# Optimization experiments

Measured on AMD Instinct MI355X. Metric: run time of the kernel, lower is better.

## Reference

```python
import jax, jax.numpy as jnp
import numpy as np

IN_F, OUT_F, RANK, ALPHA, NUM_ADAPTERS = 1024, 1024, 8, 1.0, 8
B, S = 32, 1024
SCALE = ALPHA / RANK


def setup_inputs() -> dict:
    key = jax.random.key(0)
    k1, k2, k3, k4, k5, k6 = jax.random.split(key, 6)
    x = jax.random.normal(k1, (B, S, IN_F), dtype=jnp.float32)
    subject_id = jax.random.randint(k2, (B,), 0, NUM_ADAPTERS)
    # base linear: W [out,in], bias [out] (torch nn.Linear layout)
    W = jax.random.normal(k3, (OUT_F, IN_F), dtype=jnp.float32) * (1.0 / np.sqrt(IN_F))
    b = jax.random.normal(k4, (OUT_F,), dtype=jnp.float32) * 0.01
    # stacked LoRA weights: A [E, rank, in], Bw [E, out, rank]
    # (original inits Bw to zeros; randomized here so the LoRA path is exercised)
    A = jax.random.normal(k5, (NUM_ADAPTERS, RANK, IN_F), dtype=jnp.float32) * 0.02
    Bw = jax.random.normal(k6, (NUM_ADAPTERS, OUT_F, RANK), dtype=jnp.float32) * 0.02
    return {"x": x, "W": W, "b": b, "A": A, "Bw": Bw, "subject_id": subject_id}


def reference(x, W, b, A, Bw, subject_id):
    # base linear: [B,S,O]
    out = jnp.einsum("bsd,od->bso", x, W) + b
    # gather per-batch adapter weights (equivalent to the per-adapter mask loop)
    A_sel = A[subject_id]   # [B, rank, in]
    B_sel = Bw[subject_id]  # [B, out, rank]
    h = jnp.einsum("bsd,brd->bsr", x, A_sel)          # [B,S,rank]
    lora = jnp.einsum("bsr,bor->bso", h, B_sel) * SCALE  # [B,S,out]
    return out + lora
```

## Files before the change

kernel.cpp:

```cpp
#include <hip/hip_runtime.h>
#include <hip/hip_bf16.h>

typedef __bf16 bf16_t;
typedef bf16_t bf16x4 __attribute__((ext_vector_type(4)));
typedef bf16_t bf16x8 __attribute__((ext_vector_type(8)));
typedef float  f32x4  __attribute__((ext_vector_type(4)));

#define IN_F   1024
#define OUT_F  1024
#define RANK   8
#define NE     8
#define BATCH  32
#define SEQ    1024
#define M_TOT  (BATCH * SEQ)
#define SCALE  0.125f
#define NT     16

#define GLOAD_LDS16(g, l)                                                     \
  __builtin_amdgcn_global_load_lds(                                           \
      (const __attribute__((address_space(1))) void*)(g),                     \
      (__attribute__((address_space(3))) void*)(l), 16, 0, 0)

#define CFENCE asm volatile("" ::: "memory")
#define BAR()                                                                 \
  do { CFENCE; __builtin_amdgcn_s_barrier(); CFENCE; } while (0)
#define VMCNT(n) asm volatile("s_waitcnt vmcnt(" #n ")" ::: "memory")

__global__ __launch_bounds__(256) void build_weff(
    const float* __restrict__ W, const float* __restrict__ A,
    const float* __restrict__ Bw, bf16_t* __restrict__ weff) {
  const int e  = blockIdx.x >> 10;
  const int o  = blockIdx.x & 1023;
  const int d0 = threadIdx.x << 2;

  f32x4 acc = *(const f32x4*)(W + ((size_t)o << 10) + d0);
  const float* bwr = Bw + (((size_t)e << 10) + o) * RANK;
  const float* ab  = A + (((size_t)e * RANK) << 10) + d0;
#pragma unroll
  for (int r = 0; r < RANK; ++r) {
    const float s = SCALE * bwr[r];
    const f32x4 a4 = *(const f32x4*)(ab + ((size_t)r << 10));
    acc += s * a4;
  }
  bf16x4 ov;
#pragma unroll
  for (int j = 0; j < 4; ++j) ov[j] = (bf16_t)acc[j];
  *(bf16x4*)(weff + (((size_t)e << 10) + o) * IN_F + d0) = ov;
}

__global__ __launch_bounds__(256) void cvt_x(const float* __restrict__ x,
                                             bf16_t* __restrict__ xb, int n4) {
  int i = blockIdx.x * 256 + threadIdx.x;
  const int stride = gridDim.x * 256;
  for (; i < n4; i += stride) {
    const f32x4 v = *(const f32x4*)(x + ((size_t)i << 2));
    bf16x4 o;
#pragma unroll
    for (int j = 0; j < 4; ++j) o[j] = (bf16_t)v[j];
    *(bf16x4*)(xb + ((size_t)i << 2)) = o;
  }
}

__global__ __launch_bounds__(512, 2) void gemm256(
    const bf16_t* __restrict__ xb, const bf16_t* __restrict__ weff,
    const float* __restrict__ bias, const int* __restrict__ sid,
    float* __restrict__ out) {
  __shared__ bf16_t lds[2][2][2][8192];

  const int bid0 = blockIdx.x;
  const int wgid = ((bid0 & 7) << 6) + (bid0 >> 3);
  const int mb = wgid >> 2, nb = wgid & 3;
  const int m0 = mb << 8, n0 = nb << 8;
  const int e = sid[mb >> 2];

  const int tid = threadIdx.x;
  const int lane = tid & 63, wid = tid >> 6;
  const int wm = wid >> 2, wn = wid & 3;

  const bf16_t* agbase = xb + ((size_t)m0 << 10);
  const bf16_t* bgbase = weff + ((size_t)e << 20) + ((size_t)n0 << 10);

  int soff[2];
#pragma unroll
  for (int i = 0; i < 2; ++i) {
    const int r = (wid << 5) + (i << 4) + (lane >> 2);
    const int sg = (lane & 3) ^ ((r >> 1) & 3);
    soff[i] = (r << 10) + (sg << 3);
  }

  int aoff[8], boff[4];
#pragma unroll
  for (int mi = 0; mi < 8; ++mi) {
    const int r = (wm << 7) + (mi << 4) + (lane & 15);
    const int g = (lane >> 4) ^ ((r >> 1) & 3);
    aoff[mi] = (r << 5) + (g << 3);
  }
#pragma unroll
  for (int ni = 0; ni < 4; ++ni) {
    const int r = (wn << 6) + (ni << 4) + (lane & 15);
    const int g = (lane >> 4) ^ ((r >> 1) & 3);
    boff[ni] = (r << 5) + (g << 3);
  }

  f32x4 acc[8][4] = {};

#define STAGE2(kt, kh)                                                        \
  do {                                                                        \
    bf16_t* _da = &lds[(kt) & 1][0][kh][wid << 10];                           \
    bf16_t* _db = &lds[(kt) & 1][1][kh][wid << 10];                           \
    const int _kc = ((kt) << 6) + ((kh) << 5);                                \
    GLOAD_LDS16(agbase + _kc + soff[0], _da);                                 \
    GLOAD_LDS16(agbase + _kc + soff[1], _da + 512);                           \
    GLOAD_LDS16(bgbase + _kc + soff[0], _db);                                 \
    GLOAD_LDS16(bgbase + _kc + soff[1], _db + 512);                           \
  } while (0)

#define PHASE_READS(kt, kh)                                                   \
  do {                                                                        \
    const bf16_t* _ab = &lds[(kt) & 1][0][kh][0];                             \
    const bf16_t* _bb = &lds[(kt) & 1][1][kh][0];                             \
    _Pragma("unroll") for (int mi = 0; mi < 8; ++mi)                          \
        af[mi] = *(const bf16x8*)(_ab + aoff[mi]);                            \
    _Pragma("unroll") for (int ni = 0; ni < 4; ++ni)                          \
        bfr[ni] = *(const bf16x8*)(_bb + boff[ni]);                           \
  } while (0)

#define MFMAS()                                                               \
  do {                                                                        \
    __builtin_amdgcn_s_setprio(1);                                            \
    _Pragma("unroll") for (int mi = 0; mi < 8; ++mi)                          \
        _Pragma("unroll") for (int ni = 0; ni < 4; ++ni)                      \
            acc[mi][ni] = __builtin_amdgcn_mfma_f32_16x16x32_bf16(            \
                af[mi], bfr[ni], acc[mi][ni], 0, 0, 0);                       \
    __builtin_amdgcn_s_setprio(0);                                            \
  } while (0)

  STAGE2(0, 0);
  STAGE2(0, 1);

  bf16x8 af[8], bfr[4];
  for (int j = 0; j < NT - 1; ++j) {
    VMCNT(4);
    BAR();
    PHASE_READS(j, 0);
    STAGE2(j + 1, 0);
    MFMAS();
    VMCNT(4);
    BAR();
    PHASE_READS(j, 1);
    STAGE2(j + 1, 1);
    MFMAS();
  }
  VMCNT(4);
  BAR();
  PHASE_READS(NT - 1, 0);
  MFMAS();
  VMCNT(0);
  BAR();
  PHASE_READS(NT - 1, 1);
  MFMAS();

  const int R0 = m0 + (wm << 7);
  const int C0 = n0 + (wn << 6);
  const int crow = (lane >> 4) << 2;
  const int ccol = lane & 15;
#pragma unroll
  for (int ni = 0; ni < 4; ++ni) {
    const int col = C0 + (ni << 4) + ccol;
    const float bv = bias[col];
#pragma unroll
    for (int mi = 0; mi < 8; ++mi) {
      const int row = R0 + (mi << 4) + crow;
#pragma unroll
      for (int j2 = 0; j2 < 4; ++j2)
        __builtin_nontemporal_store(acc[mi][ni][j2] + bv,
                                    &out[((size_t)(row + j2) << 10) + col]);
    }
  }
#undef STAGE2
#undef PHASE_READS
#undef MFMAS
}

__global__ __launch_bounds__(256) void lora_naive(
    const float* __restrict__ x, const float* __restrict__ W,
    const float* __restrict__ bias, const float* __restrict__ A,
    const float* __restrict__ Bw, const int* __restrict__ sid,
    float* __restrict__ out) {
  const int m = blockIdx.x;
  const int e = sid[m >> 10];
  __shared__ float xs[IN_F];
  __shared__ float h[RANK];
  const int tid = threadIdx.x;
  for (int i = tid; i < IN_F; i += 256) xs[i] = x[((size_t)m << 10) + i];
  __syncthreads();
  if (tid < RANK) {
    float s = 0.f;
    const float* ar = A + (((size_t)e * RANK + tid) << 10);
    for (int d = 0; d < IN_F; ++d) s += xs[d] * ar[d];
    h[tid] = s * SCALE;
  }
  __syncthreads();
  for (int o = tid; o < OUT_F; o += 256) {
    const float* wr = W + ((size_t)o << 10);
    float s = 0.f;
    for (int d = 0; d < IN_F; ++d) s += xs[d] * wr[d];
    const float* bwr = Bw + (((size_t)e << 10) + o) * RANK;
    float l = 0.f;
#pragma unroll
    for (int r = 0; r < RANK; ++r) l += h[r] * bwr[r];
    out[((size_t)m << 10) + o] = s + bias[o] + l;
  }
}

extern "C" void kernel_launch(void* const* d_in, const int* in_sizes, int n_in,
                              void* d_out, int out_size, void* d_ws,
                              size_t ws_size, hipStream_t stream) {
  const float* x   = (const float*)d_in[0];
  const float* W   = (const float*)d_in[1];
  const float* b   = (const float*)d_in[2];
  const float* A   = (const float*)d_in[3];
  const float* Bw  = (const float*)d_in[4];
  const int*   sid = (const int*)d_in[5];
  float* out = (float*)d_out;

  const size_t weff_bytes = (size_t)NE * OUT_F * IN_F * 2;
  const size_t xb_bytes   = (size_t)M_TOT * IN_F * 2;

  if (ws_size >= weff_bytes + xb_bytes) {
    bf16_t* weff = (bf16_t*)d_ws;
    bf16_t* xb   = (bf16_t*)((char*)d_ws + weff_bytes);
    hipLaunchKernelGGL(build_weff, dim3(NE * OUT_F), dim3(256), 0, stream,
                       W, A, Bw, weff);
    hipLaunchKernelGGL(cvt_x, dim3(4096), dim3(256), 0, stream,
                       x, xb, M_TOT * IN_F / 4);
    hipLaunchKernelGGL(gemm256, dim3((M_TOT / 256) * (OUT_F / 256)),
                       dim3(512), 0, stream, xb, weff, b, sid, out);
  } else {
    hipLaunchKernelGGL(lora_naive, dim3(M_TOT), dim3(256), 0, stream,
                       x, W, b, A, Bw, sid, out);
  }
}
```

Before: 128.3 us.

## Merge prep kernels and restructure GEMM main loop into finer-grained staged pipeline

Fuses the weight-building and x-conversion kernels into one launch, cutting one kernel launch and letting the two prep workloads overlap. The GEMM main loop is rewritten as a deeper pipeline: A and B tiles are staged separately, two tiles ahead for B, and the MFMA work is split into four sub-phases that interleave LDS reads, global-to-LDS loads and barriers. The output store changes from nontemporal to a regular store. The extra barriers and the more complex vmcnt accounting add sync overhead and a risk of mis-scheduled waits.

```diff
diff --git a/kernel.cpp b/kernel.cpp
--- a/kernel.cpp
+++ b/kernel.cpp
@@ -26,38 +26,40 @@
   do { CFENCE; __builtin_amdgcn_s_barrier(); CFENCE; } while (0)
 #define VMCNT(n) asm volatile("s_waitcnt vmcnt(" #n ")" ::: "memory")
 
-__global__ __launch_bounds__(256) void build_weff(
+__global__ __launch_bounds__(256) void prep(
     const float* __restrict__ W, const float* __restrict__ A,
-    const float* __restrict__ Bw, bf16_t* __restrict__ weff) {
-  const int e  = blockIdx.x >> 10;
-  const int o  = blockIdx.x & 1023;
-  const int d0 = threadIdx.x << 2;
-
-  f32x4 acc = *(const f32x4*)(W + ((size_t)o << 10) + d0);
-  const float* bwr = Bw + (((size_t)e << 10) + o) * RANK;
-  const float* ab  = A + (((size_t)e * RANK) << 10) + d0;
-#pragma unroll
-  for (int r = 0; r < RANK; ++r) {
-    const float s = SCALE * bwr[r];
-    const f32x4 a4 = *(const f32x4*)(ab + ((size_t)r << 10));
-    acc += s * a4;
-  }
-  bf16x4 ov;
-#pragma unroll
-  for (int j = 0; j < 4; ++j) ov[j] = (bf16_t)acc[j];
-  *(bf16x4*)(weff + (((size_t)e << 10) + o) * IN_F + d0) = ov;
-}
-
-__global__ __launch_bounds__(256) void cvt_x(const float* __restrict__ x,
-                                             bf16_t* __restrict__ xb, int n4) {
-  int i = blockIdx.x * 256 + threadIdx.x;
-  const int stride = gridDim.x * 256;
-  for (; i < n4; i += stride) {
-    const f32x4 v = *(const f32x4*)(x + ((size_t)i << 2));
-    bf16x4 o;
-#pragma unroll
-    for (int j = 0; j < 4; ++j) o[j] = (bf16_t)v[j];
-    *(bf16x4*)(xb + ((size_t)i << 2)) = o;
+    const float* __restrict__ Bw, const float* __restrict__ x,
+    bf16_t* __restrict__ weff, bf16_t* __restrict__ xb) {
+  const int bid = blockIdx.x;
+  if (bid < NE * OUT_F) {
+    const int e  = bid >> 10;
+    const int o  = bid & 1023;
+    const int d0 = threadIdx.x << 2;
+    f32x4 acc = *(const f32x4*)(W + ((size_t)o << 10) + d0);
+    const float* bwr = Bw + (((size_t)e << 10) + o) * RANK;
+    const float* ab  = A + (((size_t)e * RANK) << 10) + d0;
+#pragma unroll
+    for (int r = 0; r < RANK; ++r) {
+      const float s = SCALE * bwr[r];
+      const f32x4 a4 = *(const f32x4*)(ab + ((size_t)r << 10));
+      acc += s * a4;
+    }
+    bf16x4 ov;
+#pragma unroll
+    for (int j = 0; j < 4; ++j) ov[j] = (bf16_t)acc[j];
+    *(bf16x4*)(weff + (((size_t)e << 10) + o) * IN_F + d0) = ov;
+  } else {
+    const int cb = bid - NE * OUT_F;
+    int i = cb * 256 + threadIdx.x;
+    const int stride = 2048 * 256;
+    const int n4 = M_TOT * IN_F / 4;
+    for (; i < n4; i += stride) {
+      const f32x4 v = *(const f32x4*)(x + ((size_t)i << 2));
+      bf16x4 o;
+#pragma unroll
+      for (int j = 0; j < 4; ++j) o[j] = (bf16_t)v[j];
+      *(bf16x4*)(xb + ((size_t)i << 2)) = o;
+    }
   }
 }
 
@@ -65,7 +67,8 @@
     const bf16_t* __restrict__ xb, const bf16_t* __restrict__ weff,
     const float* __restrict__ bias, const int* __restrict__ sid,
     float* __restrict__ out) {
-  __shared__ bf16_t lds[2][2][2][8192];
+  __shared__ bf16_t lds_a[2][2][8192];
+  __shared__ bf16_t lds_b[2][2][8192];
 
   const int bid0 = blockIdx.x;
   const int wgid = ((bid0 & 7) << 6) + (bid0 >> 3);
@@ -103,62 +106,81 @@
   }
 
   f32x4 acc[8][4] = {};
-
-#define STAGE2(kt, kh)                                                        \
-  do {                                                                        \
-    bf16_t* _da = &lds[(kt) & 1][0][kh][wid << 10];                           \
-    bf16_t* _db = &lds[(kt) & 1][1][kh][wid << 10];                           \
+  bf16x8 afq[4], bf0[4], bf1[4];
+
+#define ASTG(kt, c, kh)                                                       \
+  do {                                                                        \
+    bf16_t* _d = &lds_a[c][kh][wid << 10];                                    \
     const int _kc = ((kt) << 6) + ((kh) << 5);                                \
-    GLOAD_LDS16(agbase + _kc + soff[0], _da);                                 \
-    GLOAD_LDS16(agbase + _kc + soff[1], _da + 512);                           \
-    GLOAD_LDS16(bgbase + _kc + soff[0], _db);                                 \
-    GLOAD_LDS16(bgbase + _kc + soff[1], _db + 512);                           \
-  } while (0)
-
-#define PHASE_READS(kt, kh)                                                   \
-  do {                                                                        \
-    const bf16_t* _ab = &lds[(kt) & 1][0][kh][0];                             \
-    const bf16_t* _bb = &lds[(kt) & 1][1][kh][0];                             \
-    _Pragma("unroll") for (int mi = 0; mi < 8; ++mi)                          \
-        af[mi] = *(const bf16x8*)(_ab + aoff[mi]);                            \
+    GLOAD_LDS16(agbase + _kc + soff[0], _d);                                  \
+    GLOAD_LDS16(agbase + _kc + soff[1], _d + 512);                            \
+  } while (0)
+
+#define BSTG(kt, c, kh)                                                       \
+  do {                                                                        \
+    bf16_t* _d = &lds_b[c][kh][wid << 10];                                    \
+    const int _kc = ((kt) << 6) + ((kh) << 5);                                \
+    GLOAD_LDS16(bgbase + _kc + soff[0], _d);                                  \
+    GLOAD_LDS16(bgbase + _kc + soff[1], _d + 512);                            \
+  } while (0)
+
+#define RDB(SET, c, kh)                                                       \
+  do {                                                                        \
+    const bf16_t* _bb = &lds_b[c][kh][0];                                     \
     _Pragma("unroll") for (int ni = 0; ni < 4; ++ni)                          \
-        bfr[ni] = *(const bf16x8*)(_bb + boff[ni]);                           \
-  } while (0)
-
-#define MFMAS()                                                               \
+        SET[ni] = *(const bf16x8*)(_bb + boff[ni]);                           \
+  } while (0)
+
+#define RDA(c, kh, mb_)                                                       \
+  do {                                                                        \
+    const bf16_t* _ab = &lds_a[c][kh][0];                                     \
+    _Pragma("unroll") for (int q = 0; q < 4; ++q)                             \
+        afq[q] = *(const bf16x8*)(_ab + aoff[(mb_) + q]);                     \
+  } while (0)
+
+#define MM(SET, mb_)                                                          \
   do {                                                                        \
     __builtin_amdgcn_s_setprio(1);                                            \
-    _Pragma("unroll") for (int mi = 0; mi < 8; ++mi)                          \
+    _Pragma("unroll") for (int q = 0; q < 4; ++q)                             \
         _Pragma("unroll") for (int ni = 0; ni < 4; ++ni)                      \
-            acc[mi][ni] = __builtin_amdgcn_mfma_f32_16x16x32_bf16(            \
-                af[mi], bfr[ni], acc[mi][ni], 0, 0, 0);                       \
+            acc[(mb_) + q][ni] = __builtin_amdgcn_mfma_f32_16x16x32_bf16(     \
+                afq[q], SET[ni], acc[(mb_) + q][ni], 0, 0, 0);                \
     __builtin_amdgcn_s_setprio(0);                                            \
   } while (0)
 
-  STAGE2(0, 0);
-  STAGE2(0, 1);
-
-  bf16x8 af[8], bfr[4];
-  for (int j = 0; j < NT - 1; ++j) {
-    VMCNT(4);
-    BAR();
-    PHASE_READS(j, 0);
-    STAGE2(j + 1, 0);
-    MFMAS();
-    VMCNT(4);
-    BAR();
-    PHASE_READS(j, 1);
-    STAGE2(j + 1, 1);
-    MFMAS();
-  }
-  VMCNT(4);
+#define TILE(JV, C, DO_S1, DO_S234, WTAIL)                                    \
+  do {                                                                        \
+                                                                      \
+    RDB(bf0, C, 0); RDA(C, 0, 0);                                             \
+    if (DO_S1) ASTG((JV) + 1, 1 - (C), 1);                                    \
+    BAR(); MM(bf0, 0); BAR();                                                 \
+                                                                      \
+    RDA(C, 0, 4);                                                             \
+    if (DO_S234) BSTG((JV) + 2, C, 0);                                        \
+    BAR(); MM(bf0, 4); BAR();                                                 \
+                                                                      \
+    RDB(bf1, C, 1); RDA(C, 1, 0);                                             \
+    if (DO_S234) ASTG((JV) + 2, C, 0);                                        \
+    BAR(); MM(bf1, 0); BAR();                                                 \
+                                                                      \
+    RDA(C, 1, 4);                                                             \
+    if (DO_S234) BSTG((JV) + 2, C, 1);                                        \
+    WTAIL;                                                                    \
+    BAR(); MM(bf1, 4); BAR();                                                 \
+  } while (0)
+
+  ASTG(0, 0, 0); ASTG(0, 0, 1); BSTG(0, 0, 0); BSTG(0, 0, 1);
+  BSTG(1, 1, 0); ASTG(1, 1, 0); BSTG(1, 1, 1);
+  VMCNT(6);
   BAR();
-  PHASE_READS(NT - 1, 0);
-  MFMAS();
-  VMCNT(0);
-  BAR();
-  PHASE_READS(NT - 1, 1);
-  MFMAS();
+
+  for (int jj = 0; jj < 7; ++jj) {
+    const int j0 = jj << 1;
+    TILE(j0, 0, 1, 1, VMCNT(6));
+    TILE(j0 + 1, 1, 1, 1, VMCNT(6));
+  }
+  TILE(14, 0, 1, 0, VMCNT(0));
+  TILE(15, 1, 0, 0, (void)0);
 
   const int R0 = m0 + (wm << 7);
   const int C0 = n0 + (wn << 6);
@@ -173,13 +195,15 @@
       const int row = R0 + (mi << 4) + crow;
 #pragma unroll
       for (int j2 = 0; j2 < 4; ++j2)
-        __builtin_nontemporal_store(acc[mi][ni][j2] + bv,
-                                    &out[((size_t)(row + j2) << 10) + col]);
+        out[((size_t)(row + j2) << 10) + col] = acc[mi][ni][j2] + bv;
     }
   }
-#undef STAGE2
-#undef PHASE_READS
-#undef MFMAS
+#undef ASTG
+#undef BSTG
+#undef RDB
+#undef RDA
+#undef MM
+#undef TILE
 }
 
 __global__ __launch_bounds__(256) void lora_naive(
@@ -230,10 +254,8 @@
   if (ws_size >= weff_bytes + xb_bytes) {
     bf16_t* weff = (bf16_t*)d_ws;
     bf16_t* xb   = (bf16_t*)((char*)d_ws + weff_bytes);
-    hipLaunchKernelGGL(build_weff, dim3(NE * OUT_F), dim3(256), 0, stream,
-                       W, A, Bw, weff);
-    hipLaunchKernelGGL(cvt_x, dim3(4096), dim3(256), 0, stream,
-                       x, xb, M_TOT * IN_F / 4);
+    hipLaunchKernelGGL(prep, dim3(NE * OUT_F + 2048), dim3(256), 0, stream,
+                       W, A, Bw, x, weff, xb);
     hipLaunchKernelGGL(gemm256, dim3((M_TOT / 256) * (OUT_F / 256)),
                        dim3(512), 0, stream, xb, weff, b, sid, out);
   } else {
```

After: 141.1 us. +10.0%, slower.
